# Kernel tuning notes

Hardware: AMD Instinct MI355X
Metric: run time of the kernel (lower is better)

The kernel has to match this reference:

```python
import jax, jax.numpy as jnp
import numpy as np

B, C, D, H, W = 2, 14, 96, 96, 96
WARMUP_EPOCHS = 30
CURRENT_EPOCH = 0
MAX_TOPK_RATIO = 0.3
EPS = 1e-5


def _topk_ratio():
    # mirrors get_current_topk_ratio()
    if CURRENT_EPOCH < WARMUP_EPOCHS:
        progress = CURRENT_EPOCH / WARMUP_EPOCHS
        return 0.1 + (MAX_TOPK_RATIO - 0.1) * progress
    return MAX_TOPK_RATIO


def setup_inputs() -> dict:
    key = jax.random.key(0)
    k1, k2 = jax.random.split(key)
    pred = jax.random.normal(k1, (B, C, D, H, W), dtype=jnp.float32)
    labels = jax.random.randint(k2, (B, D, H, W), 0, C)
    # one-hot ground-truth mask, class axis = 1 (matches target.view(B, C, -1))
    target = jax.nn.one_hot(labels, C, axis=1, dtype=jnp.float32)
    return {"pred": pred, "target": target}


def reference(pred, target):
    p = jax.nn.softmax(pred, axis=1).reshape(B, C, -1)  # [B, C, N]
    t = target.reshape(B, C, -1)                        # [B, C, N]
    N = p.shape[-1]
    k = max(1, int(N * _topk_ratio()))  # static k (88473 for 96^3, ratio 0.1)

    # batched top-k over abs error for every (b, c) pair at once
    err = jnp.abs(p - t)
    _, idx = jax.lax.top_k(err, k)                      # [B, C, k]
    p_k = jnp.take_along_axis(p, idx, axis=-1)
    t_k = jnp.take_along_axis(t, idx, axis=-1)

    # squared_pred=True dice on the top-k voxels
    inter = jnp.sum(p_k * p_k * t_k, axis=-1)           # [B, C]
    union = jnp.sum(p_k * p_k, axis=-1) + jnp.sum(t_k, axis=-1)
    dice = (2.0 * inter + EPS) / (union + EPS)
    loss = 1.0 - dice                                   # [B, C]

    # mask out classes with empty target (t.sum()==0 skip in the loop)
    valid = (jnp.sum(t, axis=-1) > 0).astype(p.dtype)   # [B, C]
    n_valid = jnp.sum(valid, axis=-1)                   # [B]
    per_batch = jnp.sum(loss * valid, axis=-1) / jnp.maximum(n_valid, 1.0)
    bmask = (n_valid > 0).astype(p.dtype)
    return jnp.sum(per_batch * bmask) / jnp.maximum(jnp.sum(bmask), 1.0)
```

## Files before the change

kernel.cpp:

```cpp
#include <hip/hip_runtime.h>
#include <stdint.h>

#define B_ 2
#define C_ 14
#define N_ 884736
#define K_ 88473
#define NP 28
#define M_ 27648
#define MBLK 108
#define RS_HI 2465
#define RS_LO 3065
#define CAPMAX 131072
#define EPS_ 1e-5
#define G2 864
#define CAPB 64
#define TIECAP 512
#define CCP 16
#define PS 70
#define KLDS 28672

struct Ctrl {
  double sum_p2[NP];
  double sum_p2t[NP];
  double sum_t[NP];
  double sum_tall[NP];
  double cntA[NP];
  unsigned cand_cnt[NP * CCP];
  unsigned brackets[NP * 2];
};

#define COMP(v, h) ((h) == 0 ? (v).x : (h) == 1 ? (v).y : (h) == 2 ? (v).z : (v).w)

template <int NB>
__device__ void rank_bin(const unsigned* hist, int R, unsigned* sb, int tid) {
  __shared__ unsigned wtot[4];
  const int per = NB / 256;
  const int base = tid * per;
  unsigned local = 0;
#pragma unroll
  for (int j = 0; j < per; ++j) local += hist[base + j];
  int lane = tid & 63, wv = tid >> 6;
  unsigned v = local;
#pragma unroll
  for (int o = 1; o < 64; o <<= 1) {
    unsigned w = __shfl_down(v, o);
    if (lane + o < 64) v += w;
  }
  if (lane == 0) wtot[wv] = v;
  __syncthreads();
  unsigned excl = v - local;
  for (int w2 = wv + 1; w2 < 4; ++w2) excl += wtot[w2];
  if ((int)excl < R && R <= (int)(excl + local)) {
    unsigned rem = (unsigned)R - excl;
    for (int j = per - 1; j >= 0; --j) {
      unsigned h = hist[base + j];
      if (h >= rem) { sb[0] = (unsigned)(base + j); sb[1] = rem; break; }
      rem -= h;
    }
  }
  __syncthreads();
}

__device__ unsigned select31(const unsigned* samp, int n, int R,
                             unsigned* hist, unsigned* sb, int tid) {
  for (int i = tid; i < 2048; i += 256) hist[i] = 0;
  __syncthreads();
  for (int i = tid; i < n; i += 256) atomicAdd(&hist[samp[i] >> 20], 1u);
  __syncthreads();
  rank_bin<2048>(hist, R, sb, tid);
  unsigned b1 = sb[0]; int r1 = (int)sb[1];
  __syncthreads();
  for (int i = tid; i < 2048; i += 256) hist[i] = 0;
  __syncthreads();
  for (int i = tid; i < n; i += 256) {
    unsigned kk = samp[i];
    if ((kk >> 20) == b1) atomicAdd(&hist[(kk >> 9) & 0x7FF], 1u);
  }
  __syncthreads();
  rank_bin<2048>(hist, r1, sb, tid);
  unsigned b2 = sb[0]; int r2 = (int)sb[1];
  unsigned pfx = (b1 << 11) | b2;
  __syncthreads();
  for (int i = tid; i < 512; i += 256) hist[i] = 0;
  __syncthreads();
  for (int i = tid; i < n; i += 256) {
    unsigned kk = samp[i];
    if ((kk >> 9) == pfx) atomicAdd(&hist[kk & 0x1FF], 1u);
  }
  __syncthreads();
  rank_bin<512>(hist, r2, sb, tid);
  unsigned res = (pfx << 9) | sb[0];
  __syncthreads();
  return res;
}

__global__ __launch_bounds__(256) void k1a_sample(const float* __restrict__ pred,
                                                  const float* __restrict__ targ,
                                                  unsigned* __restrict__ sampkeys) {
  int b = blockIdx.y;
  int pos = blockIdx.x * 256 + threadIdx.x;
  float x[C_], tv[C_];
#pragma unroll
  for (int c = 0; c < C_; ++c) x[c] = pred[(size_t)(b * C_ + c) * N_ + pos];
#pragma unroll
  for (int c = 0; c < C_; ++c) tv[c] = targ[(size_t)(b * C_ + c) * N_ + pos];
  float mx = x[0];
#pragma unroll
  for (int c = 1; c < C_; ++c) mx = fmaxf(mx, x[c]);
  float s = 0.f;
#pragma unroll
  for (int c = 0; c < C_; ++c) { x[c] = __expf(x[c] - mx); s += x[c]; }
  float rs = 1.0f / s;
#pragma unroll
  for (int c = 0; c < C_; ++c) {
    float err = fabsf(x[c] * rs - tv[c]);
    sampkeys[(size_t)(b * C_ + c) * M_ + pos] = __float_as_uint(err);
  }
}

__global__ __launch_bounds__(256) void k1b_bracket(const unsigned* __restrict__ sampkeys,
                                                   Ctrl* __restrict__ ctrl) {
  __shared__ unsigned samp[M_];
  __shared__ unsigned hist[2048];
  __shared__ unsigned sb[2];
  int pair = blockIdx.x;
  int tid = threadIdx.x;
  for (int i = tid; i < M_; i += 256) samp[i] = sampkeys[(size_t)pair * M_ + i];
  __syncthreads();
  unsigned khi = select31(samp, M_, RS_HI, hist, sb, tid);
  unsigned klo = select31(samp, M_, RS_LO, hist, sb, tid);
  if (tid == 0) {
    ctrl->brackets[2 * pair] = khi;
    ctrl->brackets[2 * pair + 1] = klo;
  }
  if (tid < CCP) ctrl->cand_cnt[pair * CCP + tid] = 0u;
}

__global__ __launch_bounds__(256) void k2_main(const float* __restrict__ pred,
                                               const float* __restrict__ targ,
                                               Ctrl* __restrict__ ctrl,
                                               double* __restrict__ part,
                                               unsigned* __restrict__ cand_key,
                                               unsigned* __restrict__ cand_idx,
                                               unsigned cap) {
  int b = blockIdx.y;
  int tid = threadIdx.x;
  int lane = tid & 63;
  int wv = tid >> 6;
  __shared__ unsigned s_cnt[C_], s_base[C_], s_khi[C_], s_klo[C_];
  __shared__ unsigned s_key[C_][CAPB];
  __shared__ unsigned s_idx[C_][CAPB];
  __shared__ float s_part[4][PS];

  int pr0 = b * C_;
  if (tid < C_) {
    s_khi[tid] = ctrl->brackets[2 * (pr0 + tid)];
    s_klo[tid] = ctrl->brackets[2 * (pr0 + tid) + 1];
    s_cnt[tid] = 0u;
  }
  __syncthreads();

  const size_t gbase = (size_t)b * C_ * N_;
  const int n0 = blockIdx.x * 1024 + tid * 4;

  float4 xp[C_], xt[C_];
#pragma unroll
  for (int c = 0; c < C_; ++c)
    xp[c] = *reinterpret_cast<const float4*>(pred + gbase + (size_t)c * N_ + n0);
#pragma unroll
  for (int c = 0; c < C_; ++c)
    xt[c] = *reinterpret_cast<const float4*>(targ + gbase + (size_t)c * N_ + n0);

  float4 mx = xp[0];
#pragma unroll
  for (int c = 1; c < C_; ++c) {
    mx.x = fmaxf(mx.x, xp[c].x); mx.y = fmaxf(mx.y, xp[c].y);
    mx.z = fmaxf(mx.z, xp[c].z); mx.w = fmaxf(mx.w, xp[c].w);
  }
  float4 sum; sum.x = 0.f; sum.y = 0.f; sum.z = 0.f; sum.w = 0.f;
#pragma unroll
  for (int c = 0; c < C_; ++c) {
    xp[c].x = __expf(xp[c].x - mx.x); sum.x += xp[c].x;
    xp[c].y = __expf(xp[c].y - mx.y); sum.y += xp[c].y;
    xp[c].z = __expf(xp[c].z - mx.z); sum.z += xp[c].z;
    xp[c].w = __expf(xp[c].w - mx.w); sum.w += xp[c].w;
  }
  float4 rs;
  rs.x = 1.0f / sum.x; rs.y = 1.0f / sum.y; rs.z = 1.0f / sum.z; rs.w = 1.0f / sum.w;

  float a_p2[C_], a_p2t[C_];
  unsigned a_pk[C_];
#pragma unroll
  for (int c = 0; c < C_; ++c) { a_p2[c] = 0.f; a_p2t[c] = 0.f; a_pk[c] = 0u; }

#pragma unroll
  for (int c = 0; c < C_; ++c) {
    unsigned khi = s_khi[c], klo = s_klo[c];
#pragma unroll
    for (int h = 0; h < 4; ++h) {
      float p = COMP(xp[c], h) * COMP(rs, h);
      float t = COMP(xt[c], h);
      float err = fabsf(p - t);
      unsigned eb = __float_as_uint(err);
      bool above = eb > khi;
      bool iscand = (eb > klo) && !above;
      unsigned tbit = (t > 0.5f) ? 1u : 0u;
      if (above) {
        float pp = p * p;
        a_p2[c] += pp;
        if (tbit) a_p2t[c] += pp;
      }
      a_pk[c] += (above ? (1u << 20) : 0u) + ((above && tbit) ? (1u << 10) : 0u) + tbit;
      if (iscand) {
        unsigned pos = atomicAdd(&s_cnt[c], 1u);
        unsigned key = (eb << 1) | tbit;
        if (pos < CAPB) {
          s_key[c][pos] = key;
          s_idx[c][pos] = (unsigned)(n0 + h);
        } else {
          unsigned off = atomicAdd(&ctrl->cand_cnt[(pr0 + c) * CCP], 1u);
          if (off < cap) {
            size_t cb = (size_t)(pr0 + c) * cap + off;
            cand_key[cb] = key;
            cand_idx[cb] = (unsigned)(n0 + h);
          }
        }
      }
    }
  }

#pragma unroll
  for (int c = 0; c < C_; ++c) {
    float v0 = a_p2[c], v1 = a_p2t[c];
    unsigned u2 = a_pk[c];
    for (int o = 32; o > 0; o >>= 1) {
      v0 += __shfl_down(v0, o);
      v1 += __shfl_down(v1, o);
      u2 += (unsigned)__shfl_down((int)u2, o);
    }
    if (lane == 0) {
      s_part[wv][c * 5 + 0] = v0;
      s_part[wv][c * 5 + 1] = v1;
      s_part[wv][c * 5 + 2] = (float)((u2 >> 10) & 0x3FF);
      s_part[wv][c * 5 + 3] = (float)(u2 >> 20);
      s_part[wv][c * 5 + 4] = (float)(u2 & 0x3FF);
    }
  }
  __syncthreads();

  if (tid < C_) {
    unsigned cnt = s_cnt[tid]; if (cnt > CAPB) cnt = CAPB;
    s_base[tid] = atomicAdd(&ctrl->cand_cnt[(pr0 + tid) * CCP], cnt);
  }
  if (tid < PS) {
    double v = (double)s_part[0][tid] + (double)s_part[1][tid] +
               (double)s_part[2][tid] + (double)s_part[3][tid];
    part[(size_t)(b * G2 + blockIdx.x) * PS + tid] = v;
  }
  __syncthreads();

  for (int c = 0; c < C_; ++c) {
    unsigned cnt = s_cnt[c]; if (cnt > CAPB) cnt = CAPB;
    unsigned bas = s_base[c];
    for (unsigned i = tid; i < cnt; i += 256) {
      unsigned off = bas + i;
      if (off < cap) {
        size_t cb = (size_t)(pr0 + c) * cap + off;
        cand_key[cb] = s_key[c][i];
        cand_idx[cb] = s_idx[c][i];
      }
    }
  }
}

__global__ __launch_bounds__(256) void k3_finish(Ctrl* __restrict__ ctrl,
                                                 const double* __restrict__ part,
                                                 const unsigned* __restrict__ cand_key,
                                                 const unsigned* __restrict__ cand_idx,
                                                 unsigned cap) {
  __shared__ unsigned s_keys[KLDS];
  __shared__ unsigned hist[2048];
  __shared__ unsigned sb[2];
  __shared__ double s_red5[4][5];
  __shared__ double s_sum[5];
  __shared__ unsigned s_ties[TIECAP];
  __shared__ unsigned s_tiecnt;
  __shared__ float redf[4][3];
  int pair = blockIdx.x;
  int b = pair / C_, c = pair % C_;
  int tid = threadIdx.x;
  int lane = tid & 63, wv = tid >> 6;

  double acc0 = 0, acc1 = 0, acc2 = 0, acc3 = 0, acc4 = 0;
  for (int g = tid; g < G2; g += 256) {
    const double* pp = part + (size_t)(b * G2 + g) * PS + c * 5;
    acc0 += pp[0]; acc1 += pp[1]; acc2 += pp[2]; acc3 += pp[3]; acc4 += pp[4];
  }
  for (int o = 32; o > 0; o >>= 1) {
    acc0 += __shfl_down(acc0, o); acc1 += __shfl_down(acc1, o);
    acc2 += __shfl_down(acc2, o); acc3 += __shfl_down(acc3, o);
    acc4 += __shfl_down(acc4, o);
  }
  if (lane == 0) {
    s_red5[wv][0] = acc0; s_red5[wv][1] = acc1; s_red5[wv][2] = acc2;
    s_red5[wv][3] = acc3; s_red5[wv][4] = acc4;
  }
  __syncthreads();
  if (tid == 0) {
    for (int q = 0; q < 5; ++q)
      s_sum[q] = s_red5[0][q] + s_red5[1][q] + s_red5[2][q] + s_red5[3][q];
    s_tiecnt = 0;
  }
  __syncthreads();
  double d_p2 = s_sum[0], d_p2t = s_sum[1], d_t = s_sum[2];
  double d_cnt = s_sum[3], d_tall = s_sum[4];

  unsigned nc = ctrl->cand_cnt[pair * CCP];
  if (nc > cap) nc = cap;
  int r = K_ - (int)(d_cnt + 0.5);
  if (r > (int)nc) r = (int)nc;

  double add_p2 = 0, add_p2t = 0, add_t = 0;
  if (r > 0) {
    const unsigned* gkey = cand_key + (size_t)pair * cap;
    const unsigned* gidx = cand_idx + (size_t)pair * cap;
    bool in_lds = (nc <= KLDS);
    if (in_lds)
      for (int i = tid; i < (int)nc; i += 256) s_keys[i] = gkey[i];
    __syncthreads();
    const unsigned* key = in_lds ? (const unsigned*)s_keys : gkey;

    for (int i = tid; i < 2048; i += 256) hist[i] = 0;
    __syncthreads();
    for (int i = tid; i < (int)nc; i += 256) atomicAdd(&hist[key[i] >> 21], 1u);
    __syncthreads();
    rank_bin<2048>(hist, r, sb, tid);
    unsigned b1 = sb[0]; int r1 = (int)sb[1];
    __syncthreads();
    for (int i = tid; i < 2048; i += 256) hist[i] = 0;
    __syncthreads();
    for (int i = tid; i < (int)nc; i += 256) {
      unsigned kk = key[i];
      if ((kk >> 21) == b1) atomicAdd(&hist[(kk >> 10) & 0x7FF], 1u);
    }
    __syncthreads();
    rank_bin<2048>(hist, r1, sb, tid);
    unsigned b2 = sb[0]; int r2 = (int)sb[1];
    unsigned pfx22 = (b1 << 11) | b2;
    __syncthreads();
    for (int i = tid; i < 512; i += 256) hist[i] = 0;
    __syncthreads();
    for (int i = tid; i < (int)nc; i += 256) {
      unsigned kk = key[i];
      if ((kk >> 10) == pfx22) atomicAdd(&hist[(kk >> 1) & 0x1FF], 1u);
    }
    __syncthreads();
    rank_bin<512>(hist, r2, sb, tid);
    unsigned tau = (pfx22 << 9) | sb[0];
    int need = (int)sb[1];

    float f_p2 = 0.f, f_p2t = 0.f, f_t = 0.f;
    for (int i = tid; i < (int)nc; i += 256) {
      unsigned kk = key[i];
      unsigned eb = kk >> 1;
      if (eb > tau) {
        float err = __uint_as_float(eb);
        float t = (float)(kk & 1u);
        float p = (kk & 1u) ? (1.f - err) : err;
        float pp = p * p;
        f_p2 += pp; f_p2t += pp * t; f_t += t;
      } else if (eb == tau) {
        unsigned pos = atomicAdd(&s_tiecnt, 1u);
        if (pos < TIECAP) s_ties[pos] = (gidx[i] << 1) | (kk & 1u);
      }
    }
    for (int o = 32; o > 0; o >>= 1) {
      f_p2 += __shfl_down(f_p2, o); f_p2t += __shfl_down(f_p2t, o);
      f_t += __shfl_down(f_t, o);
    }
    if (lane == 0) { redf[wv][0] = f_p2; redf[wv][1] = f_p2t; redf[wv][2] = f_t; }
    __syncthreads();

    if (tid == 0) {
      add_p2  = (double)redf[0][0] + redf[1][0] + redf[2][0] + redf[3][0];
      add_p2t = (double)redf[0][1] + redf[1][1] + redf[2][1] + redf[3][1];
      add_t   = (double)redf[0][2] + redf[1][2] + redf[2][2] + redf[3][2];
      unsigned tc = s_tiecnt; if (tc > TIECAP) tc = TIECAP;
      int take = need; if (take > (int)tc) take = (int)tc;
      float errf = __uint_as_float(tau);
      for (int s = 0; s < take; ++s) {
        unsigned best = 0xFFFFFFFFu; int bi = -1;
        for (int j = 0; j < (int)tc; ++j)
          if (s_ties[j] < best) { best = s_ties[j]; bi = j; }
        if (bi < 0) break;
        s_ties[bi] = 0xFFFFFFFFu;
        float t = (float)(best & 1u);
        float p = (best & 1u) ? (1.f - errf) : errf;
        add_p2 += (double)(p * p); add_p2t += (double)(p * p) * t; add_t += (double)t;
      }
    }
  }

  if (tid == 0) {
    ctrl->sum_p2[pair]   = d_p2 + add_p2;
    ctrl->sum_p2t[pair]  = d_p2t + add_p2t;
    ctrl->sum_t[pair]    = d_t + add_t;
    ctrl->sum_tall[pair] = d_tall;
    ctrl->cntA[pair]     = d_cnt;
  }
}

__global__ void k4_final(const Ctrl* __restrict__ ctrl, float* __restrict__ out) {
  if (threadIdx.x == 0 && blockIdx.x == 0) {
    double total = 0.0, nb = 0.0;
    for (int b = 0; b < B_; ++b) {
      double sl = 0.0, nv = 0.0;
      for (int c = 0; c < C_; ++c) {
        int pr = b * C_ + c;
        if (ctrl->sum_tall[pr] > 0.0) {
          double inter = ctrl->sum_p2t[pr];
          double uni = ctrl->sum_p2[pr] + ctrl->sum_t[pr];
          double dice = (2.0 * inter + EPS_) / (uni + EPS_);
          sl += 1.0 - dice;
          nv += 1.0;
        }
      }
      if (nv > 0.0) { total += sl / nv; nb += 1.0; }
    }
    out[0] = (float)(nb > 0.0 ? total / nb : 0.0);
  }
}

extern "C" void kernel_launch(void* const* d_in, const int* in_sizes, int n_in,
                              void* d_out, int out_size, void* d_ws, size_t ws_size,
                              hipStream_t stream) {
  const float* pred = (const float*)d_in[0];
  const float* targ = (const float*)d_in[1];
  Ctrl* ctrl = (Ctrl*)d_ws;
  double* part = (double*)((char*)d_ws + 4096);
  size_t part_bytes = (size_t)(B_ * G2) * PS * sizeof(double);
  size_t samp_off = (4096 + part_bytes + 255) & ~(size_t)255;
  unsigned* sampkeys = (unsigned*)((char*)d_ws + samp_off);
  size_t cand_off = (samp_off + (size_t)NP * M_ * 4 + 255) & ~(size_t)255;

  unsigned cap = CAPMAX;
  if (ws_size > cand_off + 1024) {
    size_t avail = (ws_size - cand_off) / (8 * NP);
    if (avail < (size_t)cap) cap = (unsigned)avail;
  } else {
    cap = 1;
  }
  unsigned* cand_key = (unsigned*)((char*)d_ws + cand_off);
  unsigned* cand_idx = cand_key + (size_t)NP * cap;
  float* out = (float*)d_out;

  k1a_sample<<<dim3(MBLK, B_), dim3(256), 0, stream>>>(pred, targ, sampkeys);
  k1b_bracket<<<dim3(NP), dim3(256), 0, stream>>>(sampkeys, ctrl);
  k2_main<<<dim3(G2, B_), dim3(256), 0, stream>>>(pred, targ, ctrl, part, cand_key, cand_idx, cap);
  k3_finish<<<dim3(NP), dim3(256), 0, stream>>>(ctrl, part, cand_key, cand_idx, cap);
  k4_final<<<dim3(1), dim3(1), 0, stream>>>(ctrl, out);
}
```

Measured before the change: 319.0 us.

## Fuse bracket selections, pack target bits, and raise k2 occupancy

The bracket kernel now finds both the high and low radix thresholds in a single pass per level, using two histograms, where before it ran two full three-level selections. This halves the scans over the shared-memory sample. In k2_main, the 14 float4 target vectors are packed into per-voxel bitmasks so they need not stay in registers. The error is computed as 1-p or p from the packed bit instead of abs(p - t), which assumes exact one-hot targets. launch_bounds(256,2) asks for two blocks per SM, and the global loads are issued before the bracket read and barrier, which may trade some register spilling for more loads in flight.

New measurement: 311.1 us. 2.5% less time.

```diff
diff --git a/kernel.cpp b/kernel.cpp
--- a/kernel.cpp
+++ b/kernel.cpp
@@ -61,39 +61,6 @@
   __syncthreads();
 }
 
-__device__ unsigned select31(const unsigned* samp, int n, int R,
-                             unsigned* hist, unsigned* sb, int tid) {
-  for (int i = tid; i < 2048; i += 256) hist[i] = 0;
-  __syncthreads();
-  for (int i = tid; i < n; i += 256) atomicAdd(&hist[samp[i] >> 20], 1u);
-  __syncthreads();
-  rank_bin<2048>(hist, R, sb, tid);
-  unsigned b1 = sb[0]; int r1 = (int)sb[1];
-  __syncthreads();
-  for (int i = tid; i < 2048; i += 256) hist[i] = 0;
-  __syncthreads();
-  for (int i = tid; i < n; i += 256) {
-    unsigned kk = samp[i];
-    if ((kk >> 20) == b1) atomicAdd(&hist[(kk >> 9) & 0x7FF], 1u);
-  }
-  __syncthreads();
-  rank_bin<2048>(hist, r1, sb, tid);
-  unsigned b2 = sb[0]; int r2 = (int)sb[1];
-  unsigned pfx = (b1 << 11) | b2;
-  __syncthreads();
-  for (int i = tid; i < 512; i += 256) hist[i] = 0;
-  __syncthreads();
-  for (int i = tid; i < n; i += 256) {
-    unsigned kk = samp[i];
-    if ((kk >> 9) == pfx) atomicAdd(&hist[kk & 0x1FF], 1u);
-  }
-  __syncthreads();
-  rank_bin<512>(hist, r2, sb, tid);
-  unsigned res = (pfx << 9) | sb[0];
-  __syncthreads();
-  return res;
-}
-
 __global__ __launch_bounds__(256) void k1a_sample(const float* __restrict__ pred,
                                                   const float* __restrict__ targ,
                                                   unsigned* __restrict__ sampkeys) {
@@ -121,14 +88,56 @@
 __global__ __launch_bounds__(256) void k1b_bracket(const unsigned* __restrict__ sampkeys,
                                                    Ctrl* __restrict__ ctrl) {
   __shared__ unsigned samp[M_];
-  __shared__ unsigned hist[2048];
+  __shared__ unsigned histH[2048], histL[2048];
   __shared__ unsigned sb[2];
   int pair = blockIdx.x;
   int tid = threadIdx.x;
   for (int i = tid; i < M_; i += 256) samp[i] = sampkeys[(size_t)pair * M_ + i];
-  __syncthreads();
-  unsigned khi = select31(samp, M_, RS_HI, hist, sb, tid);
-  unsigned klo = select31(samp, M_, RS_LO, hist, sb, tid);
+  for (int i = tid; i < 2048; i += 256) histH[i] = 0;
+  __syncthreads();
+
+  for (int i = tid; i < M_; i += 256) atomicAdd(&histH[samp[i] >> 20], 1u);
+  __syncthreads();
+  rank_bin<2048>(histH, RS_HI, sb, tid);
+  unsigned b1h = sb[0]; int r1h = (int)sb[1];
+  __syncthreads();
+  rank_bin<2048>(histH, RS_LO, sb, tid);
+  unsigned b1l = sb[0]; int r1l = (int)sb[1];
+  __syncthreads();
+
+  for (int i = tid; i < 2048; i += 256) { histH[i] = 0; histL[i] = 0; }
+  __syncthreads();
+  for (int i = tid; i < M_; i += 256) {
+    unsigned kk = samp[i];
+    unsigned top = kk >> 20;
+    if (top == b1h) atomicAdd(&histH[(kk >> 9) & 0x7FF], 1u);
+    if (top == b1l) atomicAdd(&histL[(kk >> 9) & 0x7FF], 1u);
+  }
+  __syncthreads();
+  rank_bin<2048>(histH, r1h, sb, tid);
+  unsigned b2h = sb[0]; int r2h = (int)sb[1];
+  __syncthreads();
+  rank_bin<2048>(histL, r1l, sb, tid);
+  unsigned b2l = sb[0]; int r2l = (int)sb[1];
+  unsigned pfxh = (b1h << 11) | b2h;
+  unsigned pfxl = (b1l << 11) | b2l;
+  __syncthreads();
+
+  for (int i = tid; i < 512; i += 256) { histH[i] = 0; histL[i] = 0; }
+  __syncthreads();
+  for (int i = tid; i < M_; i += 256) {
+    unsigned kk = samp[i];
+    unsigned pp = kk >> 9;
+    if (pp == pfxh) atomicAdd(&histH[kk & 0x1FF], 1u);
+    if (pp == pfxl) atomicAdd(&histL[kk & 0x1FF], 1u);
+  }
+  __syncthreads();
+  rank_bin<512>(histH, r2h, sb, tid);
+  unsigned khi = (pfxh << 9) | sb[0];
+  __syncthreads();
+  rank_bin<512>(histL, r2l, sb, tid);
+  unsigned klo = (pfxl << 9) | sb[0];
+
   if (tid == 0) {
     ctrl->brackets[2 * pair] = khi;
     ctrl->brackets[2 * pair + 1] = klo;
@@ -136,13 +145,13 @@
   if (tid < CCP) ctrl->cand_cnt[pair * CCP + tid] = 0u;
 }
 
-__global__ __launch_bounds__(256) void k2_main(const float* __restrict__ pred,
-                                               const float* __restrict__ targ,
-                                               Ctrl* __restrict__ ctrl,
-                                               double* __restrict__ part,
-                                               unsigned* __restrict__ cand_key,
-                                               unsigned* __restrict__ cand_idx,
-                                               unsigned cap) {
+__global__ __launch_bounds__(256, 2) void k2_main(const float* __restrict__ pred,
+                                                  const float* __restrict__ targ,
+                                                  Ctrl* __restrict__ ctrl,
+                                                  double* __restrict__ part,
+                                                  unsigned* __restrict__ cand_key,
+                                                  unsigned* __restrict__ cand_idx,
+                                                  unsigned cap) {
   int b = blockIdx.y;
   int tid = threadIdx.x;
   int lane = tid & 63;
@@ -153,23 +162,32 @@
   __shared__ float s_part[4][PS];
 
   int pr0 = b * C_;
+  const size_t gbase = (size_t)b * C_ * N_;
+  const int n0 = blockIdx.x * 1024 + tid * 4;
+
+  float4 xp[C_], xt[C_];
+#pragma unroll
+  for (int c = 0; c < C_; ++c) {
+    xp[c] = *reinterpret_cast<const float4*>(pred + gbase + (size_t)c * N_ + n0);
+    xt[c] = *reinterpret_cast<const float4*>(targ + gbase + (size_t)c * N_ + n0);
+  }
+
   if (tid < C_) {
     s_khi[tid] = ctrl->brackets[2 * (pr0 + tid)];
     s_klo[tid] = ctrl->brackets[2 * (pr0 + tid) + 1];
     s_cnt[tid] = 0u;
   }
-  __syncthreads();
-
-  const size_t gbase = (size_t)b * C_ * N_;
-  const int n0 = blockIdx.x * 1024 + tid * 4;
-
-  float4 xp[C_], xt[C_];
-#pragma unroll
-  for (int c = 0; c < C_; ++c)
-    xp[c] = *reinterpret_cast<const float4*>(pred + gbase + (size_t)c * N_ + n0);
-#pragma unroll
-  for (int c = 0; c < C_; ++c)
-    xt[c] = *reinterpret_cast<const float4*>(targ + gbase + (size_t)c * N_ + n0);
+
+  unsigned tb[4];
+  tb[0] = tb[1] = tb[2] = tb[3] = 0u;
+#pragma unroll
+  for (int c = 0; c < C_; ++c) {
+    if (xt[c].x > 0.5f) tb[0] |= 1u << c;
+    if (xt[c].y > 0.5f) tb[1] |= 1u << c;
+    if (xt[c].z > 0.5f) tb[2] |= 1u << c;
+    if (xt[c].w > 0.5f) tb[3] |= 1u << c;
+  }
+  __syncthreads();
 
   float4 mx = xp[0];
 #pragma unroll
@@ -199,12 +217,11 @@
 #pragma unroll
     for (int h = 0; h < 4; ++h) {
       float p = COMP(xp[c], h) * COMP(rs, h);
-      float t = COMP(xt[c], h);
-      float err = fabsf(p - t);
+      unsigned tbit = (tb[h] >> c) & 1u;
+      float err = tbit ? (1.0f - p) : p;
       unsigned eb = __float_as_uint(err);
       bool above = eb > khi;
       bool iscand = (eb > klo) && !above;
-      unsigned tbit = (t > 0.5f) ? 1u : 0u;
       if (above) {
         float pp = p * p;
         a_p2[c] += pp;
```
